# Kernel tuning notes

Measured on AMD Instinct MI355X. Metric: run time of the kernel, lower is better.

## Reference

```python
import jax, jax.numpy as jnp
import numpy as np

HEADS = 16
DIM_HEAD = 64
HEIGHT = 16
KERNEL = 5
DILATION = 1
ALPHA = 32 ** 2


def stable_softmax(t, axis=-1, alpha=ALPHA):
    t = t / alpha
    t = t - jax.lax.stop_gradient(jnp.max(t, axis=axis, keepdims=True))
    return jax.nn.softmax(t * alpha, axis=axis)


def setup_inputs() -> dict:
    key = jax.random.key(0)
    ks = jax.random.split(key, 5)
    b, n, dim = 4, 4097, 1024
    inner = HEADS * DIM_HEAD
    x = jax.random.normal(ks[0], (b, n, dim), dtype=jnp.float32)
    w_qkv = jax.random.normal(ks[1], (dim, 3 * inner), dtype=jnp.float32) * (dim ** -0.5)
    w_out = jax.random.normal(ks[2], (inner, dim), dtype=jnp.float32) * (inner ** -0.5)
    b_out = jax.random.normal(ks[3], (dim,), dtype=jnp.float32) * 0.02
    w_th = jax.random.normal(ks[4], (HEADS, HEADS), dtype=jnp.float32) * (HEADS ** -0.5)
    return {"x": x, "w_qkv": w_qkv, "w_out": w_out, "b_out": b_out, "w_th": w_th}


def reference(x, w_qkv, w_out, b_out, w_th):
    b, n, dim = x.shape
    h, d = HEADS, DIM_HEAD
    height, K, dil = HEIGHT, KERNEL, DILATION
    pad = dil * (K - 1) // 2
    scale = d ** -0.5
    kernel_numel = K * height

    # pad (n-1) non-BOS tokens to a multiple of height (static shapes)
    seq_pad = (-(n - 1)) % height
    xp = jnp.pad(x, ((0, 0), (0, seq_pad), (0, 0))) if seq_pad > 0 else x

    qkv = xp @ w_qkv  # [b, np, 3*inner]
    q, k, v = jnp.split(qkv, 3, axis=-1)

    if n == 1:  # bos-only path
        return v @ w_out + b_out

    out_bos = v[:, :1]  # [b, 1, inner]

    def to_heads(t):
        return t.reshape(b, -1, h, d).transpose(0, 2, 1, 3)  # [b,h,np,d]

    q, k, v = map(to_heads, (q, k, v))
    q = q * scale

    k_bos, k = k[:, :, 0], k[:, :, 1:]
    v_bos, v = v[:, :, 0], v[:, :, 1:]
    q = q[:, :, 1:]

    X = q.shape[2] // height  # number of timesteps

    # k, v as 2D grids [b,h,X,height,d]; unfold local windows along timestep axis
    k = k.reshape(b, h, X, height, d)
    v = v.reshape(b, h, X, height, d)
    kp = jnp.pad(k, ((0, 0), (0, 0), (pad, pad), (0, 0), (0, 0)))
    vp = jnp.pad(v, ((0, 0), (0, 0), (pad, pad), (0, 0), (0, 0)))
    idx = jnp.arange(X)[:, None] + jnp.arange(K)[None, :] * dil  # [X, K]
    kw = kp[:, :, idx].reshape(b, h, X, kernel_numel, d)  # [b,h,X,K*height,d]
    vw = vp[:, :, idx].reshape(b, h, X, kernel_numel, d)

    # prepend BOS key/value to every window
    kb = jnp.broadcast_to(k_bos[:, :, None, None, :], (b, h, X, 1, d))
    vb = jnp.broadcast_to(v_bos[:, :, None, None, :], (b, h, X, 1, d))
    kw = jnp.concatenate([kb, kw], axis=3)  # [b,h,X,1+kn,d]
    vw = jnp.concatenate([vb, vw], axis=3)

    qw = q.reshape(b, h, X, height, d)  # [b,h,X,height,d]
    sim = jnp.einsum('bhnid,bhnjd->bhnij', qw, kw)  # [b,h,X,height,1+kn]

    # causal mask over unfolded windows (BOS column never masked)
    seq_len = X * height
    q_range = jnp.arange(seq_len).reshape(X, height)
    k_range = jnp.pad(jnp.arange(seq_len).reshape(X, height), ((pad, pad), (0, 0)),
                      constant_values=seq_len)
    kr = k_range[idx].reshape(X, kernel_numel)  # [X, kn]
    mask = q_range[:, :, None] < kr[:, None, :]  # [X, height, kn]
    mask = jnp.pad(mask, ((0, 0), (0, 0), (1, 0)), constant_values=False)

    mask_value = -jnp.finfo(sim.dtype).max
    sim = jnp.where(mask[None, None], mask_value, sim)

    attn = stable_softmax(sim, axis=-1)
    # talking heads: 1x1x1 Conv3d over head channels == head mixing matmul
    attn = jnp.einsum('gh,bhnij->bgnij', w_th, attn)

    out = jnp.einsum('bhnij,bhnjd->bhnid', attn, vw)  # [b,h,X,height,d]
    out = out.transpose(0, 2, 3, 1, 4).reshape(b, X * height, h * d)
    out = jnp.concatenate([out_bos, out], axis=1)
    return (out @ w_out + b_out)[:, :n]
```

## Files before the change

### kernel.cpp

```cpp
#include <hip/hip_runtime.h>
#include <stdint.h>

typedef unsigned short u16;
typedef unsigned int u32;
typedef __attribute__((ext_vector_type(8))) short bf16x8;
typedef __attribute__((ext_vector_type(4))) float f32x4;

__device__ __forceinline__ float bf2f(u16 u) {
    union { u32 i; float f; } v; v.i = ((u32)u) << 16; return v.f;
}
__device__ __forceinline__ u16 f2bf(float f) {
    union { float f; u32 i; } v; v.f = f;
    u32 x = v.i;
    u32 r = (x + 0x7FFFu + ((x >> 16) & 1u)) >> 16;
    return (u16)r;
}

__device__ __forceinline__ void gld_lds16(const void* g, void* l) {
    __builtin_amdgcn_global_load_lds(
        (const __attribute__((address_space(1))) void*)g,
        (__attribute__((address_space(3))) void*)l, 16, 0, 0);
}

__global__ __launch_bounds__(256) void cvt_rows(
    const float* __restrict__ src, u16* __restrict__ dst, size_t total4) {
    size_t i = (size_t)blockIdx.x * 256 + threadIdx.x;
    if (i >= total4) return;
    const float4 v = ((const float4*)src)[i];
    u16 o[4] = {f2bf(v.x), f2bf(v.y), f2bf(v.z), f2bf(v.w)};
    *(unsigned long long*)(dst + i * 4) = *(unsigned long long*)o;
}

__global__ __launch_bounds__(256) void transpose_cvt(
    const float* __restrict__ src, u16* __restrict__ dst, int R, int C) {
    __shared__ float tile[32][33];
    int c0 = blockIdx.x * 32, r0 = blockIdx.y * 32;
    int tx = threadIdx.x & 31, ty = threadIdx.x >> 5;
    for (int rr = ty; rr < 32; rr += 8)
        tile[rr][tx] = src[(size_t)(r0 + rr) * C + c0 + tx];
    __syncthreads();
    for (int rr = ty; rr < 32; rr += 8)
        dst[(size_t)(c0 + rr) * R + r0 + tx] = f2bf(tile[tx][rr]);
}

template <int MODE>
__global__ __launch_bounds__(256) void gemm_bt(
    const u16* __restrict__ A, const u16* __restrict__ Bt,
    const float* __restrict__ bias, void* __restrict__ Cv,
    int M, int N, int K) {
    __shared__ u16 As[128 * 32];
    __shared__ u16 Bs[128 * 32];
    int tid = threadIdx.x;
    int wid = tid >> 6, lane = tid & 63;
    int m0 = blockIdx.x * 128, n0 = blockIdx.y * 128;
    int wr = wid >> 1, wc = wid & 1;
    int lr = lane & 15, lk = (lane >> 4) * 8;
    f32x4 acc[4][4] = {};

    for (int k0 = 0; k0 < K; k0 += 32) {
        for (int p = 0; p < 2; ++p) {
            int idx = p * 256 + tid;
            int row = idx >> 2;
            int col = (idx & 3) * 8;
            int gm = m0 + row; if (gm > M - 1) gm = M - 1;
            gld_lds16(A + (size_t)gm * K + k0 + col, As + idx * 8);
            int gn = n0 + row;
            gld_lds16(Bt + (size_t)gn * K + k0 + col, Bs + idx * 8);
        }
        __syncthreads();
        bf16x8 a[4], b[4];
        for (int mi = 0; mi < 4; ++mi)
            a[mi] = *(const bf16x8*)&As[(wr * 64 + mi * 16 + lr) * 32 + lk];
        for (int ni = 0; ni < 4; ++ni)
            b[ni] = *(const bf16x8*)&Bs[(wc * 64 + ni * 16 + lr) * 32 + lk];
        for (int mi = 0; mi < 4; ++mi)
            for (int ni = 0; ni < 4; ++ni)
                acc[mi][ni] = __builtin_amdgcn_mfma_f32_16x16x32_bf16(
                    a[mi], b[ni], acc[mi][ni], 0, 0, 0);
        __syncthreads();
    }

    int lq = lane >> 4;
    for (int mi = 0; mi < 4; ++mi)
        for (int ni = 0; ni < 4; ++ni) {
            int col = n0 + wc * 64 + ni * 16 + lr;
            float bv = (MODE == 1) ? bias[col] : 0.0f;
            for (int r = 0; r < 4; ++r) {
                int row = m0 + wr * 64 + mi * 16 + lq * 4 + r;
                if (row < M) {
                    if (MODE == 0)
                        ((u16*)Cv)[(size_t)row * N + col] = f2bf(acc[mi][ni][r]);
                    else
                        ((float*)Cv)[(size_t)row * N + col] = acc[mi][ni][r] + bv;
                }
            }
        }
}

__global__ __launch_bounds__(256) void bos_copy(
    const u16* __restrict__ qkv, u16* __restrict__ attn_out) {
    int b = blockIdx.x;
    int c = blockIdx.y * 256 + threadIdx.x;
    attn_out[(size_t)b * 4097 * 1024 + c] =
        qkv[(size_t)b * 4097 * 3072 + 2048 + c];
}

__device__ __forceinline__ int pswz(int j, int i, int h) {
    int byte = j * 512 + i * 32 + h * 2;
    int sw = ((j & 7) ^ ((j >> 3) & 7) ^ ((i >> 2) & 3)) & 7;
    return byte ^ (sw << 4);
}

__global__ __launch_bounds__(256) void attn_kernel(
    const u16* __restrict__ qkv, const float* __restrict__ w_th,
    u16* __restrict__ attn_out) {
    __shared__ u16 P[64 * 16 * 16];
    __shared__ u16 vt[4][2048];
    __shared__ float wth_s[256];

    int tid = threadIdx.x;
    int wid = tid >> 6, lane = tid & 63;
    int x = blockIdx.x;
    int b = blockIdx.y;
    size_t base = (size_t)b * 4097 * 3072;
    int lr = lane & 15;
    int lq = lane >> 4;
    int lk8 = lq * 8;

    wth_s[tid] = w_th[tid];

    for (int hh = 0; hh < 4; ++hh) {
        int h = wid * 4 + hh;
        const u16* qp = qkv + base + (size_t)(1 + x * 16 + lr) * 3072 + h * 64;
        bf16x8 aq0 = *(const bf16x8*)(qp + lk8);
        bf16x8 aq1 = *(const bf16x8*)(qp + 32 + lk8);
        f32x4 acc[4];
        #pragma unroll
        for (int jt = 0; jt < 4; ++jt) {
            int j = jt * 16 + lr;
            int tpos = x * 16 - 32 + (j - 1);
            int t = (j > 0 && tpos >= 0 && tpos < 4096) ? tpos + 1 : 0;
            const u16* kp = qkv + base + (size_t)t * 3072 + 1024 + h * 64;
            bf16x8 bk0 = *(const bf16x8*)(kp + lk8);
            bf16x8 bk1 = *(const bf16x8*)(kp + 32 + lk8);
            f32x4 c = {};
            c = __builtin_amdgcn_mfma_f32_16x16x32_bf16(aq0, bk0, c, 0, 0, 0);
            c = __builtin_amdgcn_mfma_f32_16x16x32_bf16(aq1, bk1, c, 0, 0, 0);
            acc[jt] = c;
        }
        float m[4], s[4], p[4][4];
        #pragma unroll
        for (int r = 0; r < 4; ++r) m[r] = -3.0e38f;
        #pragma unroll
        for (int jt = 0; jt < 4; ++jt) {
            int j = jt * 16 + lr;
            int tpos = x * 16 - 32 + (j - 1);
            bool jvalid = (j == 0) || (tpos >= 0);
            #pragma unroll
            for (int r = 0; r < 4; ++r) {
                int i = lq * 4 + r;
                bool keep = jvalid && (j == 0 || j <= i + 33);
                float v = keep ? acc[jt][r] * 0.125f : -3.0e38f;
                p[jt][r] = v;
                m[r] = fmaxf(m[r], v);
            }
        }
        #pragma unroll
        for (int r = 0; r < 4; ++r) {
            float v = m[r];
            v = fmaxf(v, __shfl_xor(v, 1));
            v = fmaxf(v, __shfl_xor(v, 2));
            v = fmaxf(v, __shfl_xor(v, 4));
            v = fmaxf(v, __shfl_xor(v, 8));
            m[r] = v; s[r] = 0.0f;
        }
        #pragma unroll
        for (int jt = 0; jt < 4; ++jt)
            #pragma unroll
            for (int r = 0; r < 4; ++r) {
                float e = __expf(p[jt][r] - m[r]);
                p[jt][r] = e; s[r] += e;
            }
        #pragma unroll
        for (int r = 0; r < 4; ++r) {
            float v = s[r];
            v += __shfl_xor(v, 1); v += __shfl_xor(v, 2);
            v += __shfl_xor(v, 4); v += __shfl_xor(v, 8);
            s[r] = 1.0f / v;
        }
        #pragma unroll
        for (int jt = 0; jt < 4; ++jt) {
            int j = jt * 16 + lr;
            #pragma unroll
            for (int r = 0; r < 4; ++r) {
                int i = lq * 4 + r;
                *(u16*)((char*)P + pswz(j, i, h)) = f2bf(p[jt][r] * s[r]);
            }
        }
    }
    __syncthreads();

    const u16* vtw = &vt[wid][0];
    int jloc = lane >> 1, dh = lane & 1;
    for (int gg = 0; gg < 4; ++gg) {
        int g = wid * 4 + gg;
        float wth[16];
        #pragma unroll
        for (int h2 = 0; h2 < 16; ++h2) wth[h2] = wth_s[g * 16 + h2];
        f32x4 oacc[4] = {};
        #pragma unroll
        for (int kk = 0; kk < 2; ++kk) {
            {
                int jg = kk * 32 + jloc;
                int tpos = x * 16 - 32 + (jg - 1);
                int t = (jg > 0 && tpos >= 0 && tpos < 4096) ? tpos + 1 : 0;
                const u16* src = qkv + base + (size_t)t * 3072 + 2048 + g * 64
                               + dh * 8;
                #pragma unroll
                for (int w = 0; w < 4; ++w)
                    gld_lds16(src + w * 16, &vt[wid][w * 512 + lane * 8]);
            }
            bf16x8 av;
            #pragma unroll
            for (int e = 0; e < 8; ++e) {
                int j = kk * 32 + lk8 + e;
                bf16x8 v0 = *(const bf16x8*)((const char*)P + pswz(j, lr, 0));
                bf16x8 v1 = *(const bf16x8*)((const char*)P + pswz(j, lr, 8));
                float s0 = 0.0f, s1 = 0.0f;
                #pragma unroll
                for (int h2 = 0; h2 < 8; ++h2) {
                    s0 += wth[h2]     * bf2f((u16)v0[h2]);
                    s1 += wth[h2 + 8] * bf2f((u16)v1[h2]);
                }
                av[e] = (short)f2bf(s0 + s1);
            }
            asm volatile("s_waitcnt vmcnt(0)" ::: "memory");
            #pragma unroll
            for (int dt = 0; dt < 4; ++dt) {
                bf16x8 bv;
                #pragma unroll
                for (int e = 0; e < 8; ++e)
                    bv[e] = (short)vtw[dt * 512 + (lk8 + e) * 16 + lr];
                oacc[dt] = __builtin_amdgcn_mfma_f32_16x16x32_bf16(
                    av, bv, oacc[dt], 0, 0, 0);
            }
        }
        #pragma unroll
        for (int dt = 0; dt < 4; ++dt) {
            int col = g * 64 + dt * 16 + lr;
            #pragma unroll
            for (int r = 0; r < 4; ++r) {
                int i = lq * 4 + r;
                size_t row = (size_t)b * 4097 + 1 + (size_t)x * 16 + i;
                attn_out[row * 1024 + col] = f2bf(oacc[dt][r]);
            }
        }
    }
}

extern "C" void kernel_launch(void* const* d_in, const int* in_sizes, int n_in,
                              void* d_out, int out_size, void* d_ws, size_t ws_size,
                              hipStream_t stream) {
    const float* x     = (const float*)d_in[0];
    const float* w_qkv = (const float*)d_in[1];
    const float* w_out = (const float*)d_in[2];
    const float* b_out = (const float*)d_in[3];
    const float* w_th  = (const float*)d_in[4];
    float* out = (float*)d_out;

    const int M = 4 * 4097;
    u16* qkv      = (u16*)d_ws;
    u16* wqkvT    = qkv + (size_t)M * 3072;
    u16* woutT    = wqkvT + (size_t)3072 * 1024;
    u16* xb       = woutT + (size_t)1024 * 1024;
    u16* attn_out = xb;

    transpose_cvt<<<dim3(96, 32), 256, 0, stream>>>(w_qkv, wqkvT, 1024, 3072);
    transpose_cvt<<<dim3(32, 32), 256, 0, stream>>>(w_out, woutT, 1024, 1024);

    size_t total4 = (size_t)M * 1024 / 4;
    cvt_rows<<<(int)((total4 + 255) / 256), 256, 0, stream>>>(x, xb, total4);

    int mt = (M + 127) / 128;
    gemm_bt<0><<<dim3(mt, 3072 / 128), 256, 0, stream>>>(
        xb, wqkvT, nullptr, qkv, M, 3072, 1024);

    bos_copy<<<dim3(4, 4), 256, 0, stream>>>(qkv, attn_out);
    attn_kernel<<<dim3(256, 4), 256, 0, stream>>>(qkv, w_th, attn_out);

    gemm_bt<1><<<dim3(mt, 1024 / 128), 256, 0, stream>>>(
        attn_out, woutT, b_out, out, M, 1024, 1024);
}
```

Before: 325.9 us.

## Rewrite GEMM with 256x256 tiles, double-buffered LDS, XOR swizzle and setprio

```diff
diff --git a/kernel.cpp b/kernel.cpp
--- a/kernel.cpp
+++ b/kernel.cpp
@@ -44,49 +44,92 @@
 }
 
 template <int MODE>
-__global__ __launch_bounds__(256) void gemm_bt(
+__global__ __launch_bounds__(512) void gemm_bt2(
     const u16* __restrict__ A, const u16* __restrict__ Bt,
     const float* __restrict__ bias, void* __restrict__ Cv,
     int M, int N, int K) {
-    __shared__ u16 As[128 * 32];
-    __shared__ u16 Bs[128 * 32];
+    __shared__ u16 lds[2][2][256 * 64];
     int tid = threadIdx.x;
     int wid = tid >> 6, lane = tid & 63;
-    int m0 = blockIdx.x * 128, n0 = blockIdx.y * 128;
-    int wr = wid >> 1, wc = wid & 1;
-    int lr = lane & 15, lk = (lane >> 4) * 8;
-    f32x4 acc[4][4] = {};
-
-    for (int k0 = 0; k0 < K; k0 += 32) {
-        for (int p = 0; p < 2; ++p) {
-            int idx = p * 256 + tid;
-            int row = idx >> 2;
-            int col = (idx & 3) * 8;
-            int gm = m0 + row; if (gm > M - 1) gm = M - 1;
-            gld_lds16(A + (size_t)gm * K + k0 + col, As + idx * 8);
-            int gn = n0 + row;
-            gld_lds16(Bt + (size_t)gn * K + k0 + col, Bs + idx * 8);
-        }
-        __syncthreads();
-        bf16x8 a[4], b[4];
-        for (int mi = 0; mi < 4; ++mi)
-            a[mi] = *(const bf16x8*)&As[(wr * 64 + mi * 16 + lr) * 32 + lk];
-        for (int ni = 0; ni < 4; ++ni)
-            b[ni] = *(const bf16x8*)&Bs[(wc * 64 + ni * 16 + lr) * 32 + lk];
-        for (int mi = 0; mi < 4; ++mi)
-            for (int ni = 0; ni < 4; ++ni)
-                acc[mi][ni] = __builtin_amdgcn_mfma_f32_16x16x32_bf16(
-                    a[mi], b[ni], acc[mi][ni], 0, 0, 0);
-        __syncthreads();
+    int lr = lane & 15, lq = lane >> 4;
+    int wr = wid >> 2, wc = wid & 3;
+    int m0 = blockIdx.x * 256, n0 = blockIdx.y * 256;
+    int NT = K >> 6;
+
+    f32x4 acc[8][4] = {};
+
+    #define STAGE(t, buf)                                                     \
+    do {                                                                      \
+        int k0 = (t) << 6;                                                    \
+        _Pragma("unroll")                                                     \
+        for (int w = 0; w < 4; ++w) {                                         \
+            int g = w * 512 + tid;                                            \
+            int row = g >> 3;                                                 \
+            int cdat = (g & 7) ^ ((row & 7) ^ ((row >> 3) & 1));              \
+            int gm = m0 + row; if (gm >= M) gm = M - 1;                       \
+            gld_lds16(A + (size_t)gm * K + k0 + cdat * 8,                     \
+                      &lds[buf][0][g * 8]);                                   \
+        }                                                                     \
+        _Pragma("unroll")                                                     \
+        for (int w = 0; w < 4; ++w) {                                         \
+            int g = w * 512 + tid;                                            \
+            int row = g >> 3;                                                 \
+            int cdat = (g & 7) ^ ((row & 7) ^ ((row >> 3) & 1));              \
+            int gn = n0 + row;                                                \
+            gld_lds16(Bt + (size_t)gn * K + k0 + cdat * 8,                    \
+                      &lds[buf][1][g * 8]);                                   \
+        }                                                                     \
+    } while (0)
+
+    STAGE(0, 0);
+    STAGE(1, 1);
+
+    for (int t = 0; t < NT; ++t) {
+        int buf = t & 1;
+        if (t + 1 < NT) asm volatile("s_waitcnt vmcnt(8)" ::: "memory");
+        else            asm volatile("s_waitcnt vmcnt(0)" ::: "memory");
+        asm volatile("s_barrier" ::: "memory");
+        const u16* Ab = &lds[buf][0][0];
+        const u16* Bb = &lds[buf][1][0];
+        #pragma unroll
+        for (int ks = 0; ks < 2; ++ks) {
+            int c = ks * 4 + lq;
+            bf16x8 a[8], b[4];
+            #pragma unroll
+            for (int mi = 0; mi < 8; ++mi) {
+                int r = wr * 128 + mi * 16 + lr;
+                int cs = c ^ ((r & 7) ^ ((r >> 3) & 1));
+                a[mi] = *(const bf16x8*)&Ab[r * 64 + cs * 8];
+            }
+            #pragma unroll
+            for (int ni = 0; ni < 4; ++ni) {
+                int r = wc * 64 + ni * 16 + lr;
+                int cs = c ^ ((r & 7) ^ ((r >> 3) & 1));
+                b[ni] = *(const bf16x8*)&Bb[r * 64 + cs * 8];
+            }
+            __builtin_amdgcn_s_setprio(1);
+            #pragma unroll
+            for (int mi = 0; mi < 8; ++mi)
+                #pragma unroll
+                for (int ni = 0; ni < 4; ++ni)
+                    acc[mi][ni] = __builtin_amdgcn_mfma_f32_16x16x32_bf16(
+                        a[mi], b[ni], acc[mi][ni], 0, 0, 0);
+            __builtin_amdgcn_s_setprio(0);
+        }
+        asm volatile("s_barrier" ::: "memory");
+        if (t + 2 < NT) STAGE(t + 2, buf);
     }
-
-    int lq = lane >> 4;
-    for (int mi = 0; mi < 4; ++mi)
+    #undef STAGE
+
+    #pragma unroll
+    for (int mi = 0; mi < 8; ++mi)
+        #pragma unroll
         for (int ni = 0; ni < 4; ++ni) {
             int col = n0 + wc * 64 + ni * 16 + lr;
             float bv = (MODE == 1) ? bias[col] : 0.0f;
-            for (int r = 0; r < 4; ++r) {
-                int row = m0 + wr * 64 + mi * 16 + lq * 4 + r;
+            #pragma unroll
+            for (int r = 0; r < 4; ++r) {
+                int row = m0 + wr * 128 + mi * 16 + lq * 4 + r;
                 if (row < M) {
                     if (MODE == 0)
                         ((u16*)Cv)[(size_t)row * N + col] = f2bf(acc[mi][ni][r]);
@@ -281,13 +324,13 @@
     size_t total4 = (size_t)M * 1024 / 4;
     cvt_rows<<<(int)((total4 + 255) / 256), 256, 0, stream>>>(x, xb, total4);
 
-    int mt = (M + 127) / 128;
-    gemm_bt<0><<<dim3(mt, 3072 / 128), 256, 0, stream>>>(
+    int mt = (M + 255) / 256;
+    gemm_bt2<0><<<dim3(mt, 3072 / 256), 512, 0, stream>>>(
         xb, wqkvT, nullptr, qkv, M, 3072, 1024);
 
     bos_copy<<<dim3(4, 4), 256, 0, stream>>>(qkv, attn_out);
     attn_kernel<<<dim3(256, 4), 256, 0, stream>>>(qkv, w_th, attn_out);
 
-    gemm_bt<1><<<dim3(mt, 1024 / 128), 256, 0, stream>>>(
+    gemm_bt2<1><<<dim3(mt, 1024 / 256), 512, 0, stream>>>(
         attn_out, woutT, b_out, out, M, 1024, 1024);
 }
```

New measurement: 305.8 us. -6.2%, faster.

## Double-buffer GEMM LDS loads with swizzle, prefetch depth two, N-major grid

Applied to the files above, without the earlier changes.

```diff
diff --git a/kernel.cpp b/kernel.cpp
--- a/kernel.cpp
+++ b/kernel.cpp
@@ -44,47 +44,85 @@
 }
 
 template <int MODE>
-__global__ __launch_bounds__(256) void gemm_bt(
+__global__ __launch_bounds__(256, 3) void gemm_bt4(
     const u16* __restrict__ A, const u16* __restrict__ Bt,
     const float* __restrict__ bias, void* __restrict__ Cv,
     int M, int N, int K) {
-    __shared__ u16 As[128 * 32];
-    __shared__ u16 Bs[128 * 32];
+    __shared__ u16 Asb[2][128 * 32];
+    __shared__ u16 Bsb[2][128 * 32];
     int tid = threadIdx.x;
     int wid = tid >> 6, lane = tid & 63;
-    int m0 = blockIdx.x * 128, n0 = blockIdx.y * 128;
+    int lr = lane & 15, lq = lane >> 4;
     int wr = wid >> 1, wc = wid & 1;
-    int lr = lane & 15, lk = (lane >> 4) * 8;
+    int n0 = blockIdx.x * 128, m0 = blockIdx.y * 128;
+    int NT = K >> 5;
     f32x4 acc[4][4] = {};
 
-    for (int k0 = 0; k0 < K; k0 += 32) {
-        for (int p = 0; p < 2; ++p) {
-            int idx = p * 256 + tid;
-            int row = idx >> 2;
-            int col = (idx & 3) * 8;
-            int gm = m0 + row; if (gm > M - 1) gm = M - 1;
-            gld_lds16(A + (size_t)gm * K + k0 + col, As + idx * 8);
-            int gn = n0 + row;
-            gld_lds16(Bt + (size_t)gn * K + k0 + col, Bs + idx * 8);
-        }
-        __syncthreads();
+    #define ST_A(u, t, bi)                                                   \
+    do {                                                                     \
+        int g = (u) * 256 + tid;                                             \
+        int row = g >> 2;                                                    \
+        int c = (g & 3) ^ ((row >> 1) & 3);                                  \
+        int gm = m0 + row; if (gm >= M) gm = M - 1;                          \
+        gld_lds16(A + (size_t)gm * K + ((t) << 5) + c * 8,                   \
+                  &Asb[bi][g * 8]);                                          \
+    } while (0)
+    #define ST_B(u, t, bi)                                                   \
+    do {                                                                     \
+        int g = (u) * 256 + tid;                                             \
+        int row = g >> 2;                                                    \
+        int c = (g & 3) ^ ((row >> 1) & 3);                                  \
+        gld_lds16(Bt + (size_t)(n0 + row) * K + ((t) << 5) + c * 8,          \
+                  &Bsb[bi][g * 8]);                                          \
+    } while (0)
+
+    ST_A(0, 0, 0); ST_A(1, 0, 0); ST_B(0, 0, 0); ST_B(1, 0, 0);
+    ST_A(0, 1, 1); ST_A(1, 1, 1); ST_B(0, 1, 1); ST_B(1, 1, 1);
+
+    for (int t = 0; t < NT; ++t) {
+        int bi = t & 1;
+        if (t + 1 < NT) asm volatile("s_waitcnt vmcnt(4)" ::: "memory");
+        else            asm volatile("s_waitcnt vmcnt(0)" ::: "memory");
+        asm volatile("s_barrier" ::: "memory");
+        const u16* Ab = &Asb[bi][0];
+        const u16* Bb = &Bsb[bi][0];
         bf16x8 a[4], b[4];
+        #pragma unroll
+        for (int mi = 0; mi < 4; ++mi) {
+            int r = wr * 64 + mi * 16 + lr;
+            int cs = lq ^ ((r >> 1) & 3);
+            a[mi] = *(const bf16x8*)&Ab[r * 32 + cs * 8];
+        }
+        #pragma unroll
+        for (int ni = 0; ni < 4; ++ni) {
+            int r = wc * 64 + ni * 16 + lr;
+            int cs = lq ^ ((r >> 1) & 3);
+            b[ni] = *(const bf16x8*)&Bb[r * 32 + cs * 8];
+        }
+        __builtin_amdgcn_s_setprio(1);
+        #pragma unroll
         for (int mi = 0; mi < 4; ++mi)
-            a[mi] = *(const bf16x8*)&As[(wr * 64 + mi * 16 + lr) * 32 + lk];
-        for (int ni = 0; ni < 4; ++ni)
-            b[ni] = *(const bf16x8*)&Bs[(wc * 64 + ni * 16 + lr) * 32 + lk];
-        for (int mi = 0; mi < 4; ++mi)
+            #pragma unroll
             for (int ni = 0; ni < 4; ++ni)
                 acc[mi][ni] = __builtin_amdgcn_mfma_f32_16x16x32_bf16(
                     a[mi], b[ni], acc[mi][ni], 0, 0, 0);
-        __syncthreads();
+        __builtin_amdgcn_s_setprio(0);
+        asm volatile("s_barrier" ::: "memory");
+        if (t + 2 < NT) {
+            ST_A(0, t + 2, bi); ST_A(1, t + 2, bi);
+            ST_B(0, t + 2, bi); ST_B(1, t + 2, bi);
+        }
     }
-
-    int lq = lane >> 4;
+    #undef ST_A
+    #undef ST_B
+
+    #pragma unroll
     for (int mi = 0; mi < 4; ++mi)
+        #pragma unroll
         for (int ni = 0; ni < 4; ++ni) {
             int col = n0 + wc * 64 + ni * 16 + lr;
             float bv = (MODE == 1) ? bias[col] : 0.0f;
+            #pragma unroll
             for (int r = 0; r < 4; ++r) {
                 int row = m0 + wr * 64 + mi * 16 + lq * 4 + r;
                 if (row < M) {
@@ -282,12 +320,12 @@
     cvt_rows<<<(int)((total4 + 255) / 256), 256, 0, stream>>>(x, xb, total4);
 
     int mt = (M + 127) / 128;
-    gemm_bt<0><<<dim3(mt, 3072 / 128), 256, 0, stream>>>(
+    gemm_bt4<0><<<dim3(3072 / 128, mt), 256, 0, stream>>>(
         xb, wqkvT, nullptr, qkv, M, 3072, 1024);
 
     bos_copy<<<dim3(4, 4), 256, 0, stream>>>(qkv, attn_out);
     attn_kernel<<<dim3(256, 4), 256, 0, stream>>>(qkv, w_th, attn_out);
 
-    gemm_bt<1><<<dim3(mt, 1024 / 128), 256, 0, stream>>>(
+    gemm_bt4<1><<<dim3(1024 / 128, mt), 256, 0, stream>>>(
         attn_out, woutT, b_out, out, M, 1024, 1024);
 }
```

Result: faster. 286.2 us (-12.2%).
